# Optimization experiments

Measured on AMD Instinct MI355X. Metric: run time of the kernel, lower is better.

Reference implementation:

```python
import jax, jax.numpy as jnp
import numpy as np

GAMMA = 0.5

def _rbf_gram(a, b):
    # exp(-gamma * ||a - b||^2), computed via the expanded quadratic form.
    # a: [N, d], b: [M, d] -> [N, M]
    a2 = jnp.sum(a * a, axis=-1)                      # [N]
    b2 = jnp.sum(b * b, axis=-1)                      # [M]
    sq = a2[:, None] + b2[None, :] - 2.0 * (a @ b.T)  # [N, M]
    return jnp.exp(-GAMMA * jnp.maximum(sq, 0.0))


def setup_inputs() -> dict:
    key = jax.random.key(0)
    kx, kp = jax.random.split(key)
    x = jax.random.normal(kx, (32768, 16), dtype=jnp.float32)
    particles = jax.random.normal(kp, (8192, 16), dtype=jnp.float32)
    return {"x": x, "particles": particles}


def reference(x, particles):
    n_p = particles.shape[0]
    # p=None, norm=True -> px = ones(N_x) / N_x
    px = jnp.ones(x.shape[0], dtype=x.dtype) / x.shape[0]
    t1 = jnp.mean(_rbf_gram(particles, particles))           # mean over [N_p, N_p]
    t2 = 2.0 * jnp.sum(px @ _rbf_gram(x, particles)) / n_p   # weighted row-sum of [N_x, N_p]
    return t1 - t2
```

## Files before the change

### kernel.cpp

```cpp
#include <hip/hip_runtime.h>
#include <hip/hip_bf16.h>

#define THREADS 256
#define DIM 16

typedef __attribute__((ext_vector_type(8))) short bf16x8;
typedef __attribute__((ext_vector_type(16))) float f32x16;
typedef __attribute__((ext_vector_type(2))) float f32x2;

__device__ __forceinline__ float rawexp2(float a) { return __builtin_amdgcn_exp2f(a); }

__global__ __launch_bounds__(THREADS) void prep_kernel(
    const float* __restrict__ x, int nx,
    const float* __restrict__ p, int np,
    short* __restrict__ xbs, float* __restrict__ xn,
    short* __restrict__ pbs, short* __restrict__ pb, float* __restrict__ pn)
{
    const float L2E  = 1.44269504088896340736f;
    const float HL2E = 0.72134752044448170368f;
    int i = blockIdx.x * THREADS + threadIdx.x;
    const float* src; short* ds; short* dp; float* dn;
    if (i < nx) {
        src = x + (size_t)i * DIM; ds = xbs + (size_t)i * DIM; dp = nullptr; dn = xn + i;
    } else if (i < nx + np) {
        int j = i - nx;
        src = p + (size_t)j * DIM; ds = pbs + (size_t)j * DIM; dp = pb + (size_t)j * DIM; dn = pn + j;
    } else {
        return;
    }

    float nrm = 0.f;
    bf16x8 plo, phi, slo, shi;
#pragma unroll
    for (int k = 0; k < DIM; ++k) {
        unsigned u = __float_as_uint(src[k]);
        unsigned short r = (unsigned short)((u + 0x7FFFu + ((u >> 16) & 1u)) >> 16);
        float fr = __uint_as_float((unsigned)r << 16);
        nrm = fmaf(fr, fr, nrm);
        unsigned us = __float_as_uint(L2E * fr);
        unsigned short rs = (unsigned short)((us + 0x7FFFu + ((us >> 16) & 1u)) >> 16);
        if (k < 8) { plo[k] = (short)r; slo[k] = (short)rs; }
        else       { phi[k - 8] = (short)r; shi[k - 8] = (short)rs; }
    }
    *(bf16x8*)ds = slo; *((bf16x8*)ds + 1) = shi;
    if (dp) { *(bf16x8*)dp = plo; *((bf16x8*)dp + 1) = phi; }
    *dn = -HL2E * nrm;
}

__device__ __forceinline__ float gram_phase(
    const short* __restrict__ rowsb, const float* __restrict__ rown,
    const short* __restrict__ colsb, const float* __restrict__ coln,
    int row0, int ct0, int ntiles, int l31, int half)
{
    bf16x8 afrag = *(const bf16x8*)(rowsb + (size_t)(row0 + l31) * DIM + half * 8);

    f32x16 cseed;
#pragma unroll
    for (int r = 0; r < 16; ++r) {
        int rrow = (r & 3) + 8 * (r >> 2) + 4 * half;
        cseed[r] = rown[row0 + rrow];
    }

    f32x2 acca = {0.f, 0.f}, accb = {0.f, 0.f};
    const short* bptr = colsb + ((size_t)ct0 * 32 + l31) * DIM + half * 8;
    const float* nptr = coln + ct0 * 32 + l31;

    for (int t = 0; t < ntiles; t += 2) {
#pragma unroll
        for (int u = 0; u < 2; ++u) {
            bf16x8 bfrag = *(const bf16x8*)(bptr + (size_t)(t + u) * 32 * DIM);
            float pf = rawexp2(nptr[(t + u) * 32]);
            f32x16 d = __builtin_amdgcn_mfma_f32_32x32x16_bf16(afrag, bfrag, cseed, 0, 0, 0);
            f32x2 pf2 = {pf, pf};
#pragma unroll
            for (int r = 0; r < 8; ++r) {
                f32x2 e = { rawexp2(d[2 * r]), rawexp2(d[2 * r + 1]) };
                if (r & 1) accb = e * pf2 + accb;
                else       acca = e * pf2 + acca;
            }
        }
    }
    f32x2 s = acca + accb;
    return s.x + s.y;
}

__global__ __launch_bounds__(THREADS) void gram_fused_kernel(
    const short* __restrict__ xbs, const float* __restrict__ xn,
    const short* __restrict__ pbs, const short* __restrict__ pb,
    const float* __restrict__ pn,
    int nrt_p, int n1,
    int nrt_x, int n2,
    double sc1, double sc2,
    double* __restrict__ partials)
{
    const int lane = threadIdx.x & 63;
    const int wv   = threadIdx.x >> 6;
    const int l31  = lane & 31;
    const int half = lane >> 5;
    const int w    = blockIdx.x * (THREADS / 64) + wv;

    const int rt1 = w & (nrt_p - 1);
    const int c10 = (w / nrt_p) * n1;
    float acc1 = gram_phase(pbs, pn, pb, pn, rt1 * 32, c10, n1, l31, half);

    const int rt2 = w & (nrt_x - 1);
    const int c20 = (w / nrt_x) * n2;
    float acc2 = gram_phase(xbs, xn, pb, pn, rt2 * 32, c20, n2, l31, half);

    double v = (double)acc1 * sc1 - (double)acc2 * sc2;
#pragma unroll
    for (int off = 32; off > 0; off >>= 1) v += __shfl_down(v, off);

    __shared__ double sred[THREADS / 64];
    if (lane == 0) sred[wv] = v;
    __syncthreads();
    if (threadIdx.x == 0) {
        double tot = 0.0;
#pragma unroll
        for (int q = 0; q < THREADS / 64; ++q) tot += sred[q];
        partials[blockIdx.x] = tot;
    }
}

__global__ __launch_bounds__(THREADS) void finalize_kernel(
    const double* __restrict__ partials, int n, float* __restrict__ out)
{
    double v = 0.0;
    for (int i = threadIdx.x; i < n; i += THREADS) v += partials[i];
#pragma unroll
    for (int off = 32; off > 0; off >>= 1) v += __shfl_down(v, off);

    __shared__ double sred[THREADS / 64];
    const int lane = threadIdx.x & 63;
    const int wid = threadIdx.x >> 6;
    if (lane == 0) sred[wid] = v;
    __syncthreads();
    if (threadIdx.x == 0) {
        double tot = 0.0;
#pragma unroll
        for (int q = 0; q < THREADS / 64; ++q) tot += sred[q];
        out[0] = (float)tot;
    }
}

extern "C" void kernel_launch(void* const* d_in, const int* in_sizes, int n_in,
                              void* d_out, int out_size, void* d_ws, size_t ws_size,
                              hipStream_t stream) {
    const float* x = (const float*)d_in[0];
    const float* particles = (const float*)d_in[1];
    float* out = (float*)d_out;

    const int NX = in_sizes[0] / DIM;
    const int NP = in_sizes[1] / DIM;

    const int nrt_x = NX / 32;
    const int nrt_p = NP / 32;

    const int NBLOCKS = 2048;
    const int WAVES = NBLOCKS * (THREADS / 64);
    const int n1 = (nrt_p * nrt_p) / WAVES;
    const int n2 = (nrt_x * nrt_p) / WAVES;

    char* ws = (char*)d_ws;
    double* partials = (double*)ws;
    float*  xn  = (float*)(ws + 16384);
    float*  pn  = (float*)(ws + 147456);
    short*  xbs = (short*)(ws + 180224);
    short*  pbs = (short*)(ws + 1228800);
    short*  pb  = (short*)(ws + 1490944);

    const int nprep = (NX + NP + THREADS - 1) / THREADS;
    prep_kernel<<<nprep, THREADS, 0, stream>>>(x, NX, particles, NP, xbs, xn, pbs, pb, pn);

    gram_fused_kernel<<<NBLOCKS, THREADS, 0, stream>>>(
        xbs, xn, pbs, pb, pn,
        nrt_p, n1, nrt_x, n2,
        1.0 / ((double)NP * (double)NP),
        2.0 / ((double)NX * (double)NP),
        partials);

    finalize_kernel<<<1, THREADS, 0, stream>>>(partials, NBLOCKS, out);
}
```

Before: 54.39 us.

## Software-pipeline MFMA with exp reduction and precompute column exp factors

Precomputes the per-particle exp2 norm factor once in the prep kernel instead of recomputing it per tile per lane. The gram loop is restructured so the next tile's fragment is prefetched and its MFMA issued while the exp2 sums of the previous tile are computed. The per-element multiply by the column factor is also replaced by summing the exponentials first and applying a single fma per tile. This aims to hide MFMA latency and load latency behind transcendental work and to cut VALU ops, at the cost of extra registers for the in-flight accumulator and a slightly different summation order.

```diff
diff --git a/kernel.cpp b/kernel.cpp
--- a/kernel.cpp
+++ b/kernel.cpp
@@ -6,7 +6,6 @@
 
 typedef __attribute__((ext_vector_type(8))) short bf16x8;
 typedef __attribute__((ext_vector_type(16))) float f32x16;
-typedef __attribute__((ext_vector_type(2))) float f32x2;
 
 __device__ __forceinline__ float rawexp2(float a) { return __builtin_amdgcn_exp2f(a); }
 
@@ -14,17 +13,20 @@
     const float* __restrict__ x, int nx,
     const float* __restrict__ p, int np,
     short* __restrict__ xbs, float* __restrict__ xn,
-    short* __restrict__ pbs, short* __restrict__ pb, float* __restrict__ pn)
+    short* __restrict__ pbs, short* __restrict__ pb,
+    float* __restrict__ pn, float* __restrict__ pfp)
 {
     const float L2E  = 1.44269504088896340736f;
     const float HL2E = 0.72134752044448170368f;
     int i = blockIdx.x * THREADS + threadIdx.x;
-    const float* src; short* ds; short* dp; float* dn;
+    const float* src; short* ds; short* dp; float* dn; float* df;
     if (i < nx) {
-        src = x + (size_t)i * DIM; ds = xbs + (size_t)i * DIM; dp = nullptr; dn = xn + i;
+        src = x + (size_t)i * DIM; ds = xbs + (size_t)i * DIM;
+        dp = nullptr; dn = xn + i; df = nullptr;
     } else if (i < nx + np) {
         int j = i - nx;
-        src = p + (size_t)j * DIM; ds = pbs + (size_t)j * DIM; dp = pb + (size_t)j * DIM; dn = pn + j;
+        src = p + (size_t)j * DIM; ds = pbs + (size_t)j * DIM;
+        dp = pb + (size_t)j * DIM; dn = pn + j; df = pfp + j;
     } else {
         return;
     }
@@ -44,12 +46,14 @@
     }
     *(bf16x8*)ds = slo; *((bf16x8*)ds + 1) = shi;
     if (dp) { *(bf16x8*)dp = plo; *((bf16x8*)dp + 1) = phi; }
-    *dn = -HL2E * nrm;
+    float ns = -HL2E * nrm;
+    *dn = ns;
+    if (df) *df = rawexp2(ns);
 }
 
 __device__ __forceinline__ float gram_phase(
     const short* __restrict__ rowsb, const float* __restrict__ rown,
-    const short* __restrict__ colsb, const float* __restrict__ coln,
+    const short* __restrict__ colsb, const float* __restrict__ colpf,
     int row0, int ct0, int ntiles, int l31, int half)
 {
     bf16x8 afrag = *(const bf16x8*)(rowsb + (size_t)(row0 + l31) * DIM + half * 8);
@@ -61,33 +65,57 @@
         cseed[r] = rown[row0 + rrow];
     }
 
-    f32x2 acca = {0.f, 0.f}, accb = {0.f, 0.f};
     const short* bptr = colsb + ((size_t)ct0 * 32 + l31) * DIM + half * 8;
-    const float* nptr = coln + ct0 * 32 + l31;
-
-    for (int t = 0; t < ntiles; t += 2) {
-#pragma unroll
-        for (int u = 0; u < 2; ++u) {
-            bf16x8 bfrag = *(const bf16x8*)(bptr + (size_t)(t + u) * 32 * DIM);
-            float pf = rawexp2(nptr[(t + u) * 32]);
-            f32x16 d = __builtin_amdgcn_mfma_f32_32x32x16_bf16(afrag, bfrag, cseed, 0, 0, 0);
-            f32x2 pf2 = {pf, pf};
-#pragma unroll
-            for (int r = 0; r < 8; ++r) {
-                f32x2 e = { rawexp2(d[2 * r]), rawexp2(d[2 * r + 1]) };
-                if (r & 1) accb = e * pf2 + accb;
-                else       acca = e * pf2 + acca;
-            }
+    const float* fptr = colpf + ct0 * 32 + l31;
+    const size_t bstride = (size_t)32 * DIM;
+
+    bf16x8 bcur = *(const bf16x8*)bptr;
+    float  fcur = *fptr;
+    bf16x8 bnxt = *(const bf16x8*)(bptr + bstride);
+    float  fnxt = fptr[32];
+
+    f32x16 d = __builtin_amdgcn_mfma_f32_32x32x16_bf16(afrag, bcur, cseed, 0, 0, 0);
+    float fuse = fcur;
+
+    float acc0 = 0.f, acc1 = 0.f;
+
+#pragma unroll 2
+    for (int t = 1; t < ntiles; ++t) {
+        int tn = (t + 1 < ntiles) ? t + 1 : t;
+        bcur = bnxt; fcur = fnxt;
+        bnxt = *(const bf16x8*)(bptr + (size_t)tn * bstride);
+        fnxt = fptr[tn * 32];
+
+        f32x16 dn = __builtin_amdgcn_mfma_f32_32x32x16_bf16(afrag, bcur, cseed, 0, 0, 0);
+
+        float s0 = 0.f, s1 = 0.f;
+#pragma unroll
+        for (int r = 0; r < 16; r += 2) {
+            s0 += rawexp2(d[r]);
+            s1 += rawexp2(d[r + 1]);
         }
-    }
-    f32x2 s = acca + accb;
-    return s.x + s.y;
+        acc0 = fmaf(fuse, s0, acc0);
+        acc1 = fmaf(fuse, s1, acc1);
+
+        d = dn; fuse = fcur;
+    }
+    {
+        float s0 = 0.f, s1 = 0.f;
+#pragma unroll
+        for (int r = 0; r < 16; r += 2) {
+            s0 += rawexp2(d[r]);
+            s1 += rawexp2(d[r + 1]);
+        }
+        acc0 = fmaf(fuse, s0, acc0);
+        acc1 = fmaf(fuse, s1, acc1);
+    }
+    return acc0 + acc1;
 }
 
 __global__ __launch_bounds__(THREADS) void gram_fused_kernel(
     const short* __restrict__ xbs, const float* __restrict__ xn,
     const short* __restrict__ pbs, const short* __restrict__ pb,
-    const float* __restrict__ pn,
+    const float* __restrict__ pn, const float* __restrict__ pfp,
     int nrt_p, int n1,
     int nrt_x, int n2,
     double sc1, double sc2,
@@ -101,11 +129,11 @@
 
     const int rt1 = w & (nrt_p - 1);
     const int c10 = (w / nrt_p) * n1;
-    float acc1 = gram_phase(pbs, pn, pb, pn, rt1 * 32, c10, n1, l31, half);
+    float acc1 = gram_phase(pbs, pn, pb, pfp, rt1 * 32, c10, n1, l31, half);
 
     const int rt2 = w & (nrt_x - 1);
     const int c20 = (w / nrt_x) * n2;
-    float acc2 = gram_phase(xbs, xn, pb, pn, rt2 * 32, c20, n2, l31, half);
+    float acc2 = gram_phase(xbs, xn, pb, pfp, rt2 * 32, c20, n2, l31, half);
 
     double v = (double)acc1 * sc1 - (double)acc2 * sc2;
 #pragma unroll
@@ -165,15 +193,17 @@
     double* partials = (double*)ws;
     float*  xn  = (float*)(ws + 16384);
     float*  pn  = (float*)(ws + 147456);
-    short*  xbs = (short*)(ws + 180224);
-    short*  pbs = (short*)(ws + 1228800);
-    short*  pb  = (short*)(ws + 1490944);
+    float*  pfp = (float*)(ws + 180224);
+    short*  xbs = (short*)(ws + 212992);
+    short*  pbs = (short*)(ws + 1261568);
+    short*  pb  = (short*)(ws + 1523712);
 
     const int nprep = (NX + NP + THREADS - 1) / THREADS;
-    prep_kernel<<<nprep, THREADS, 0, stream>>>(x, NX, particles, NP, xbs, xn, pbs, pb, pn);
+    prep_kernel<<<nprep, THREADS, 0, stream>>>(x, NX, particles, NP,
+                                               xbs, xn, pbs, pb, pn, pfp);
 
     gram_fused_kernel<<<NBLOCKS, THREADS, 0, stream>>>(
-        xbs, xn, pbs, pb, pn,
+        xbs, xn, pbs, pb, pn, pfp,
         nrt_p, n1, nrt_x, n2,
         1.0 / ((double)NP * (double)NP),
         2.0 / ((double)NX * (double)NP),
```

New measurement: 51.96 us. 1.05x faster.
